# Kernel tuning notes

Hardware: AMD Instinct MI355X
Metric: run time of the kernel (lower is better)

The kernel has to match this reference:

```python
import math
import jax, jax.numpy as jnp
import numpy as np

B, S, E, H, DK, NW = 2048, 1, 1024, 128, 8, 8  # d_k == n_wires == 8, seq_len must be 1
DIM = 2 ** NW


def setup_inputs() -> dict:
    key = jax.random.key(0)
    ks = jax.random.split(key, 7)
    scale = 1.0 / math.sqrt(E)
    return {
        "x": jax.random.normal(ks[0], (B, S, E), jnp.float32),
        "wq": jax.random.normal(ks[1], (E, E), jnp.float32) * scale,
        "wk": jax.random.normal(ks[2], (E, E), jnp.float32) * scale,
        "wv": jax.random.normal(ks[3], (E, E), jnp.float32) * scale,
        "wc": jax.random.normal(ks[4], (E, E), jnp.float32) * scale,
        "bc": jax.random.normal(ks[5], (E,), jnp.float32) * 0.01,
        "rx_params": jax.random.normal(ks[6], (NW,), jnp.float32),  # trainable RX angles (shared q_layer)
    }


def _apply_rx(state, theta, wire):
    # state: (N, 2,...,2) [NW qubit axes]; theta: scalar or (N,)
    N = state.shape[0]
    theta = jnp.broadcast_to(theta, (N,))
    c = jnp.cos(theta * 0.5).astype(jnp.complex64)[:, None]
    s = (-1j * jnp.sin(theta * 0.5).astype(jnp.complex64))[:, None]
    st = jnp.moveaxis(state, wire + 1, 1).reshape(N, 2, -1)
    new = jnp.stack([c * st[:, 0] + s * st[:, 1],
                     s * st[:, 0] + c * st[:, 1]], axis=1)
    return jnp.moveaxis(new.reshape((N,) + (2,) * NW), 1, wire + 1)


def _apply_cnot(state, ctrl, tgt):
    st = jnp.moveaxis(state, (ctrl + 1, tgt + 1), (1, 2))
    st = jnp.stack([st[:, 0], jnp.flip(st[:, 1], axis=1)], axis=1)
    return jnp.moveaxis(st, (1, 2), (ctrl + 1, tgt + 1))


def _qlayer(angles, rx_params):
    # angles: (N, NW) per-sample RX encoder angles; rx_params: (NW,) shared trainable RX
    N = angles.shape[0]
    state = jnp.zeros((N,) + (2,) * NW, jnp.complex64)
    state = state.at[(slice(None),) + (0,) * NW].set(1.0 + 0j)  # |0...0>
    for w in range(NW):
        state = _apply_rx(state, angles[:, w], w)      # encoder RX(x_w)
    for w in range(NW):
        state = _apply_rx(state, rx_params[w], w)      # trainable RX
    for w in range(NW - 1):
        state = _apply_cnot(state, w, w + 1)           # CNOT chain
    state = _apply_cnot(state, NW - 1, 0)              # ring closure
    probs = jnp.abs(state.reshape(N, DIM)) ** 2
    bits = (jnp.arange(DIM)[:, None] >> jnp.arange(NW - 1, -1, -1)[None, :]) & 1  # wire 0 = MSB
    signs = (1.0 - 2.0 * bits).astype(jnp.float32)     # (DIM, NW)
    return probs @ signs                               # <Z_w> per wire, (N, NW)


def reference(x, wq, wk, wv, wc, bc, rx_params):
    q = jnp.einsum('bse,fe->bsf', x, wq).reshape(B, S, H, DK)
    k = jnp.einsum('bse,fe->bsf', x, wk).reshape(B, S, H, DK)
    v = jnp.einsum('bse,fe->bsf', x, wv).reshape(B, S, H, DK)
    scores = jnp.einsum('bqhd,bkhd->bhqk', q, k) / math.sqrt(DK)
    attn = jax.nn.softmax(scores, axis=-1)             # dropout is identity in eval
    out = jnp.einsum('bhqk,bkhd->bqhd', attn, v).reshape(B, S, E)
    # per-head quantum circuit (S==1, d_k==NW); batch all heads together
    angles = out.reshape(B * H, DK)
    qout = _qlayer(angles, rx_params).reshape(B, S, E)
    return jnp.einsum('bse,fe->bsf', qout, wc) + bc
```

## Files before the change

### kernel.cpp

```cpp
#include <hip/hip_runtime.h>
#include <hip/hip_bf16.h>
#include <math.h>


#define BB 2048
#define EN 1024

typedef short s16x8 __attribute__((ext_vector_type(8)));
typedef float f32x4 __attribute__((ext_vector_type(4)));

union Frag { s16x8 v; __hip_bfloat16 h[8]; };

__device__ inline s16x8 cvt_frag(f32x4 lo, f32x4 hi) {
    Frag u;
    #pragma unroll
    for (int j = 0; j < 4; ++j) {
        u.h[j]     = __float2bfloat16(lo[j]);
        u.h[4 + j] = __float2bfloat16(hi[j]);
    }
    return u.v;
}

__device__ inline void gll16(const __hip_bfloat16* g, __hip_bfloat16* l) {
    __builtin_amdgcn_global_load_lds(
        (const __attribute__((address_space(1))) void*)g,
        (__attribute__((address_space(3))) void*)l,
        16, 0, 0);
}

__global__ __launch_bounds__(256) void cvt3_kernel(
        const float* __restrict__ x, const float* __restrict__ wv,
        const float* __restrict__ wc,
        __hip_bfloat16* __restrict__ xb, __hip_bfloat16* __restrict__ wvb,
        __hip_bfloat16* __restrict__ wcb)
{
    const int g = blockIdx.x * 256 + threadIdx.x;
    const int NX = (BB * EN) / 8;
    const int NG = (EN * EN) / 8;
    const float* s; __hip_bfloat16* d; size_t off;
    if (g < NX)           { s = x;  d = xb;  off = (size_t)g * 8; }
    else if (g < NX + NG) { s = wv; d = wvb; off = (size_t)(g - NX) * 8; }
    else                  { s = wc; d = wcb; off = (size_t)(g - NX - NG) * 8; }
    f32x4 lo = *(const f32x4*)(s + off);
    f32x4 hi = *(const f32x4*)(s + off + 4);
    *(s16x8*)(d + off) = cvt_frag(lo, hi);
}

template <int EPI>
__global__ __launch_bounds__(512, 4) void gemm_kernel(
        const __hip_bfloat16* __restrict__ A,
        const __hip_bfloat16* __restrict__ W,
        const float* __restrict__ bias, const float* __restrict__ rx,
        void* __restrict__ Cv)
{
    __shared__ __align__(16) unsigned char smem[65536];
    __hip_bfloat16* lds = (__hip_bfloat16*)smem;

    const int tid  = threadIdx.x;
    const int wave = tid >> 6, lane = tid & 63;
    const int l15 = lane & 15, lq = lane >> 4;
    const int m0 = blockIdx.x * 64, n0 = blockIdx.y * 64;
    const int wk  = wave >> 2;
    const int wmn = wave & 3;
    const int wm  = wmn >> 1;
    const int wn  = wmn & 1;

    const __hip_bfloat16* gsrc[2];
    int ldst[2];
    #pragma unroll
    for (int i = 0; i < 2; ++i) {
        const int t = wave * 2 + i;
        int row, lofs;
        const __hip_bfloat16* base;
        if (t < 8) { const int mt = t >> 1; row = m0 + mt * 16 + l15; base = A; lofs = t * 512; }
        else       { const int u = t - 8;   row = n0 + (u >> 1) * 16 + l15; base = W; lofs = 4096 + u * 512; }
        gsrc[i] = base + (size_t)row * EN + (t & 1) * 32 + lq * 8;
        ldst[i] = lofs;
    }

    f32x4 acc[2][2] = {};

    #pragma unroll
    for (int i = 0; i < 2; ++i) gll16(gsrc[i], &lds[ldst[i]]);
    #pragma unroll
    for (int i = 0; i < 2; ++i) gll16(gsrc[i] + 64, &lds[8192 + ldst[i]]);

    #pragma unroll
    for (int k = 0; k < 16; ++k) {
        if (k < 15) asm volatile("s_waitcnt vmcnt(2)" ::: "memory");
        else        asm volatile("s_waitcnt vmcnt(0)" ::: "memory");
        __builtin_amdgcn_s_barrier();
        __builtin_amdgcn_sched_barrier(0);
        if (k + 2 < 16) {
            const int qb = ((k + 2) % 3) * 8192;
            #pragma unroll
            for (int i = 0; i < 2; ++i)
                gll16(gsrc[i] + (k + 2) * 64, &lds[qb + ldst[i]]);
        }
        const __hip_bfloat16* Ab = &lds[(k % 3) * 8192];
        const __hip_bfloat16* Bb = Ab + 4096;
        s16x8 a[2], b[2];
        #pragma unroll
        for (int mi = 0; mi < 2; ++mi)
            a[mi] = *(const s16x8*)&Ab[((wm * 2 + mi) * 2 + wk) * 512 + lane * 8];
        #pragma unroll
        for (int nj = 0; nj < 2; ++nj)
            b[nj] = *(const s16x8*)&Bb[((wn * 2 + nj) * 2 + wk) * 512 + lane * 8];
        #pragma unroll
        for (int mi = 0; mi < 2; ++mi) {
            #pragma unroll
            for (int nj = 0; nj < 2; ++nj)
                acc[mi][nj] = __builtin_amdgcn_mfma_f32_16x16x32_bf16(
                    a[mi], b[nj], acc[mi][nj], 0, 0, 0);
        }
    }

    float* red = (float*)(smem + 49152);
    if (wk == 1) {
        #pragma unroll
        for (int mi = 0; mi < 2; ++mi) {
            #pragma unroll
            for (int nj = 0; nj < 2; ++nj)
                *(f32x4*)&red[((wmn * 2 + mi) * 2 + nj) * 256 + lane * 4] = acc[mi][nj];
        }
    }
    __syncthreads();

    if (EPI == 0) {
        float* sb = (float*)smem;
        if (wk == 0) {
            #pragma unroll
            for (int mi = 0; mi < 2; ++mi) {
                #pragma unroll
                for (int nj = 0; nj < 2; ++nj) {
                    f32x4 o = *(const f32x4*)&red[((wmn * 2 + mi) * 2 + nj) * 256 + lane * 4];
                    const int col = wn * 32 + nj * 16 + l15;
                    #pragma unroll
                    for (int r = 0; r < 4; ++r)
                        sb[(wm * 32 + mi * 16 + lq * 4 + r) * 68 + col] = acc[mi][nj][r] + o[r];
                }
            }
        }
        __syncthreads();
        const int row = tid >> 3, g = tid & 7;
        const float* pv = &sb[row * 68 + g * 8];
        float t[8];
        #pragma unroll
        for (int j = 0; j < 8; ++j) t[j] = __cosf(pv[j] + rx[j]);
        Frag o;
        float suf = t[1];
        #pragma unroll
        for (int j = 2; j < 8; ++j) suf *= t[j];
        o.h[0] = __float2bfloat16(suf);
        float pr = t[0];
        #pragma unroll
        for (int j = 1; j < 8; ++j) { pr *= t[j]; o.h[j] = __float2bfloat16(pr); }
        __hip_bfloat16* V = (__hip_bfloat16*)Cv;
        *(s16x8*)(V + (size_t)(m0 + row) * EN + n0 + g * 8) = o.v;
    } else {
        if (wk == 0) {
            float* C = (float*)Cv;
            #pragma unroll
            for (int mi = 0; mi < 2; ++mi) {
                #pragma unroll
                for (int nj = 0; nj < 2; ++nj) {
                    f32x4 o = *(const f32x4*)&red[((wmn * 2 + mi) * 2 + nj) * 256 + lane * 4];
                    const int col = n0 + wn * 32 + nj * 16 + l15;
                    const float bv = bias[col];
                    #pragma unroll
                    for (int r = 0; r < 4; ++r) {
                        const int row = m0 + wm * 16 * 2 + mi * 16 + lq * 4 + r;
                        C[(size_t)row * EN + col] = acc[mi][nj][r] + o[r] + bv;
                    }
                }
            }
        }
    }
}

extern "C" void kernel_launch(void* const* d_in, const int* in_sizes, int n_in,
                              void* d_out, int out_size, void* d_ws, size_t ws_size,
                              hipStream_t stream)
{
    const float* x  = (const float*)d_in[0];
    const float* wv = (const float*)d_in[3];
    const float* wc = (const float*)d_in[4];
    const float* bc = (const float*)d_in[5];
    const float* rx = (const float*)d_in[6];
    float* out = (float*)d_out;

    const size_t XE = (size_t)BB * EN;
    const size_t WE = (size_t)EN * EN;

    __hip_bfloat16* xb  = (__hip_bfloat16*)d_ws;
    __hip_bfloat16* wvb = xb + XE;
    __hip_bfloat16* wcb = wvb + WE;
    __hip_bfloat16* V   = wcb + WE;

    dim3 grid(BB / 64, EN / 64);
    cvt3_kernel<<<(int)((XE / 8 + 2 * (WE / 8)) / 256), 256, 0, stream>>>(
        x, wv, wc, xb, wvb, wcb);
    gemm_kernel<0><<<grid, 512, 0, stream>>>(xb, wvb, nullptr, rx, V);
    gemm_kernel<1><<<grid, 512, 0, stream>>>(V, wcb, bc, nullptr, out);
}
```

Before: 114.6 us.

## Fuse fp32-to-bf16 conversion into first GEMM and drop separate convert kernel

Removes the standalone conversion kernel. The first GEMM now loads fp32 x and wv directly, converts them to bf16 in registers and stores them to LDS, using register-prefetched double buffering and no split-K. The same kernel also converts one slice of wc to bf16 per block for the second GEMM. This saves a launch and the bf16 round trip through global memory, but it gives up the async global_load_lds path, reads twice as many bytes per tile in the first GEMM, and re-reads fp32 x and wv across tiles.

After: 122.8 us. 1.07x slower.

```diff
diff --git a/kernel.cpp b/kernel.cpp
--- a/kernel.cpp
+++ b/kernel.cpp
@@ -7,9 +7,11 @@
 #define EN 1024
 
 typedef short s16x8 __attribute__((ext_vector_type(8)));
+typedef short s16x4 __attribute__((ext_vector_type(4)));
 typedef float f32x4 __attribute__((ext_vector_type(4)));
 
-union Frag { s16x8 v; __hip_bfloat16 h[8]; };
+union Frag  { s16x8 v; __hip_bfloat16 h[8]; };
+union Half4 { s16x4 v; __hip_bfloat16 h[4]; };
 
 __device__ inline s16x8 cvt_frag(f32x4 lo, f32x4 hi) {
     Frag u;
@@ -28,30 +30,119 @@
         16, 0, 0);
 }
 
-__global__ __launch_bounds__(256) void cvt3_kernel(
-        const float* __restrict__ x, const float* __restrict__ wv,
+__global__ __launch_bounds__(512, 4) void gemm1_kernel(
+        const float* __restrict__ A,
+        const float* __restrict__ W,
         const float* __restrict__ wc,
-        __hip_bfloat16* __restrict__ xb, __hip_bfloat16* __restrict__ wvb,
-        __hip_bfloat16* __restrict__ wcb)
+        const float* __restrict__ rx,
+        __hip_bfloat16* __restrict__ wcb,
+        __hip_bfloat16* __restrict__ V)
 {
-    const int g = blockIdx.x * 256 + threadIdx.x;
-    const int NX = (BB * EN) / 8;
-    const int NG = (EN * EN) / 8;
-    const float* s; __hip_bfloat16* d; size_t off;
-    if (g < NX)           { s = x;  d = xb;  off = (size_t)g * 8; }
-    else if (g < NX + NG) { s = wv; d = wvb; off = (size_t)(g - NX) * 8; }
-    else                  { s = wc; d = wcb; off = (size_t)(g - NX - NG) * 8; }
-    f32x4 lo = *(const f32x4*)(s + off);
-    f32x4 hi = *(const f32x4*)(s + off + 4);
-    *(s16x8*)(d + off) = cvt_frag(lo, hi);
-}
-
-template <int EPI>
-__global__ __launch_bounds__(512, 4) void gemm_kernel(
+    __shared__ __align__(16) unsigned char smem[33792];
+    __hip_bfloat16* lds = (__hip_bfloat16*)smem;
+
+    const int tid  = threadIdx.x;
+    const int wave = tid >> 6, lane = tid & 63;
+    const int l15 = lane & 15, lq = lane >> 4;
+    const int m0 = blockIdx.x * 64, n0 = blockIdx.y * 64;
+    const int wmt = wave >> 1;
+    const int wnt = wave & 1;
+
+    const float* gsrc[2];
+    int ldst[2];
+    #pragma unroll
+    for (int i = 0; i < 2; ++i) {
+        const int t = wave * 2 + i;
+        int row, lofs;
+        const float* base;
+        if (t < 8) { const int mt = t >> 1; row = m0 + mt * 16 + l15; base = A; lofs = t * 512; }
+        else       { const int u = t - 8;   row = n0 + (u >> 1) * 16 + l15; base = W; lofs = 4096 + u * 512; }
+        gsrc[i] = base + (size_t)row * EN + (t & 1) * 32 + lq * 8;
+        ldst[i] = lofs + lane * 8;
+    }
+
+    f32x4 acc[2] = {};
+
+    {
+        f32x4 l0 = *(const f32x4*)(gsrc[0]);
+        f32x4 h0 = *(const f32x4*)(gsrc[0] + 4);
+        f32x4 l1 = *(const f32x4*)(gsrc[1]);
+        f32x4 h1 = *(const f32x4*)(gsrc[1] + 4);
+        *(s16x8*)&lds[ldst[0]] = cvt_frag(l0, h0);
+        *(s16x8*)&lds[ldst[1]] = cvt_frag(l1, h1);
+    }
+    __syncthreads();
+
+    int p = 0;
+    for (int k0 = 64; k0 <= EN; k0 += 64) {
+        f32x4 l0, h0, l1, h1;
+        const bool pref = (k0 < EN);
+        if (pref) {
+            l0 = *(const f32x4*)(gsrc[0] + k0);
+            h0 = *(const f32x4*)(gsrc[0] + k0 + 4);
+            l1 = *(const f32x4*)(gsrc[1] + k0);
+            h1 = *(const f32x4*)(gsrc[1] + k0 + 4);
+        }
+        const __hip_bfloat16* Ab = &lds[p * 8192];
+        const __hip_bfloat16* Bb = Ab + 4096;
+        #pragma unroll
+        for (int kt = 0; kt < 2; ++kt) {
+            s16x8 a = *(const s16x8*)&Ab[(wmt * 2 + kt) * 512 + lane * 8];
+            #pragma unroll
+            for (int j = 0; j < 2; ++j) {
+                s16x8 b = *(const s16x8*)&Bb[((wnt * 2 + j) * 2 + kt) * 512 + lane * 8];
+                acc[j] = __builtin_amdgcn_mfma_f32_16x16x32_bf16(a, b, acc[j], 0, 0, 0);
+            }
+        }
+        if (pref) {
+            const int q = p ^ 1;
+            *(s16x8*)&lds[q * 8192 + ldst[0]] = cvt_frag(l0, h0);
+            *(s16x8*)&lds[q * 8192 + ldst[1]] = cvt_frag(l1, h1);
+        }
+        __syncthreads();
+        p ^= 1;
+    }
+
+    {
+        const int bf = blockIdx.y * gridDim.x + blockIdx.x;
+        const size_t co = ((size_t)bf * 512 + tid) * 4;
+        f32x4 w4 = *(const f32x4*)(wc + co);
+        Half4 hh;
+        #pragma unroll
+        for (int j = 0; j < 4; ++j) hh.h[j] = __float2bfloat16(w4[j]);
+        *(s16x4*)(wcb + co) = hh.v;
+    }
+
+    float* sb = (float*)smem;
+    #pragma unroll
+    for (int j = 0; j < 2; ++j) {
+        const int col = wnt * 32 + j * 16 + l15;
+        #pragma unroll
+        for (int r = 0; r < 4; ++r)
+            sb[(wmt * 16 + lq * 4 + r) * 68 + col] = acc[j][r];
+    }
+    __syncthreads();
+    const int row = tid >> 3, g = tid & 7;
+    const float* pv = &sb[row * 68 + g * 8];
+    float t[8];
+    #pragma unroll
+    for (int j = 0; j < 8; ++j) t[j] = __cosf(pv[j] + rx[j]);
+    Frag o;
+    float suf = t[1];
+    #pragma unroll
+    for (int j = 2; j < 8; ++j) suf *= t[j];
+    o.h[0] = __float2bfloat16(suf);
+    float pr = t[0];
+    #pragma unroll
+    for (int j = 1; j < 8; ++j) { pr *= t[j]; o.h[j] = __float2bfloat16(pr); }
+    *(s16x8*)(V + (size_t)(m0 + row) * EN + n0 + g * 8) = o.v;
+}
+
+__global__ __launch_bounds__(512, 4) void gemm2_kernel(
         const __hip_bfloat16* __restrict__ A,
         const __hip_bfloat16* __restrict__ W,
-        const float* __restrict__ bias, const float* __restrict__ rx,
-        void* __restrict__ Cv)
+        const float* __restrict__ bias,
+        float* __restrict__ C)
 {
     __shared__ __align__(16) unsigned char smem[65536];
     __hip_bfloat16* lds = (__hip_bfloat16*)smem;
@@ -126,52 +217,18 @@
     }
     __syncthreads();
 
-    if (EPI == 0) {
-        float* sb = (float*)smem;
-        if (wk == 0) {
-            #pragma unroll
-            for (int mi = 0; mi < 2; ++mi) {
+    if (wk == 0) {
+        #pragma unroll
+        for (int mi = 0; mi < 2; ++mi) {
+            #pragma unroll
+            for (int nj = 0; nj < 2; ++nj) {
+                f32x4 o = *(const f32x4*)&red[((wmn * 2 + mi) * 2 + nj) * 256 + lane * 4];
+                const int col = n0 + wn * 32 + nj * 16 + l15;
+                const float bv = bias[col];
                 #pragma unroll
-                for (int nj = 0; nj < 2; ++nj) {
-                    f32x4 o = *(const f32x4*)&red[((wmn * 2 + mi) * 2 + nj) * 256 + lane * 4];
-                    const int col = wn * 32 + nj * 16 + l15;
-                    #pragma unroll
-                    for (int r = 0; r < 4; ++r)
-                        sb[(wm * 32 + mi * 16 + lq * 4 + r) * 68 + col] = acc[mi][nj][r] + o[r];
-                }
-            }
-        }
-        __syncthreads();
-        const int row = tid >> 3, g = tid & 7;
-        const float* pv = &sb[row * 68 + g * 8];
-        float t[8];
-        #pragma unroll
-        for (int j = 0; j < 8; ++j) t[j] = __cosf(pv[j] + rx[j]);
-        Frag o;
-        float suf = t[1];
-        #pragma unroll
-        for (int j = 2; j < 8; ++j) suf *= t[j];
-        o.h[0] = __float2bfloat16(suf);
-        float pr = t[0];
-        #pragma unroll
-        for (int j = 1; j < 8; ++j) { pr *= t[j]; o.h[j] = __float2bfloat16(pr); }
-        __hip_bfloat16* V = (__hip_bfloat16*)Cv;
-        *(s16x8*)(V + (size_t)(m0 + row) * EN + n0 + g * 8) = o.v;
-    } else {
-        if (wk == 0) {
-            float* C = (float*)Cv;
-            #pragma unroll
-            for (int mi = 0; mi < 2; ++mi) {
-                #pragma unroll
-                for (int nj = 0; nj < 2; ++nj) {
-                    f32x4 o = *(const f32x4*)&red[((wmn * 2 + mi) * 2 + nj) * 256 + lane * 4];
-                    const int col = n0 + wn * 32 + nj * 16 + l15;
-                    const float bv = bias[col];
-                    #pragma unroll
-                    for (int r = 0; r < 4; ++r) {
-                        const int row = m0 + wm * 16 * 2 + mi * 16 + lq * 4 + r;
-                        C[(size_t)row * EN + col] = acc[mi][nj][r] + o[r] + bv;
-                    }
+                for (int r = 0; r < 4; ++r) {
+                    const int row = m0 + wm * 32 + mi * 16 + lq * 4 + r;
+                    C[(size_t)row * EN + col] = acc[mi][nj][r] + o[r] + bv;
                 }
             }
         }
@@ -189,17 +246,12 @@
     const float* rx = (const float*)d_in[6];
     float* out = (float*)d_out;
 
-    const size_t XE = (size_t)BB * EN;
     const size_t WE = (size_t)EN * EN;
 
-    __hip_bfloat16* xb  = (__hip_bfloat16*)d_ws;
-    __hip_bfloat16* wvb = xb + XE;
-    __hip_bfloat16* wcb = wvb + WE;
+    __hip_bfloat16* wcb = (__hip_bfloat16*)d_ws;
     __hip_bfloat16* V   = wcb + WE;
 
     dim3 grid(BB / 64, EN / 64);
-    cvt3_kernel<<<(int)((XE / 8 + 2 * (WE / 8)) / 256), 256, 0, stream>>>(
-        x, wv, wc, xb, wvb, wcb);
-    gemm_kernel<0><<<grid, 512, 0, stream>>>(xb, wvb, nullptr, rx, V);
-    gemm_kernel<1><<<grid, 512, 0, stream>>>(V, wcb, bc, nullptr, out);
-}
+    gemm1_kernel<<<grid, 512, 0, stream>>>(x, wv, wc, rx, wcb, V);
+    gemm2_kernel<<<grid, 512, 0, stream>>>(V, wcb, bc, out);
+}
```
